# Kernel optimization log

Hardware: AMD Instinct MI355X
Metric: run time of the kernel (lower is better)

Reference implementation:

```python
import jax, jax.numpy as jnp
import numpy as np

EPS = 1e-6                                   # VN leaky-relu denominator eps
BN_SCALE = np.float32(1.0 / np.sqrt(1.0 + 1e-5))  # eval-mode BatchNorm with default stats
NEG = 0.2                                    # negative_slope


def vn_lin(x, w):
    # x: [n, c, 3, ...]; w: [c, o] -> [n, o, 3, ...]
    return jnp.einsum('nc...,co->no...', x, w)


def vn_act(p, d):
    # Vector-Neuron leaky ReLU: project p off the half-space defined by direction d.
    dot = jnp.sum(p * d, axis=2, keepdims=True)
    dsq = jnp.sum(d * d, axis=2, keepdims=True)
    corr = p - (dot / (dsq + EPS)) * d
    return NEG * p + (1.0 - NEG) * jnp.where(dot >= 0, p, corr)


def score_net(x, w_vn, wd_vn, w_h1, w_h2, b_h2, temp=1.0):
    # CorrelationNet: VNLinearLeakyReLU(3 -> 2*ks) -> norm -> 1x1 convs -> softmax
    p = vn_lin(x, w_vn) * BN_SCALE           # [N, 2ks, 3, K] (VNBatchNorm ~ scalar in eval)
    d = vn_lin(x, wd_vn)
    s = vn_act(p, d)
    s = jnp.linalg.norm(s, axis=2)           # [N, 2ks, K]
    s = jax.nn.relu(jnp.einsum('nck,co->nok', s, w_h1) * BN_SCALE)  # conv1d k=1, BN, relu
    s = jnp.einsum('nck,co->nok', s, w_h2) + b_h2[None, :, None]     # last conv with bias
    return jax.nn.softmax(s / temp, axis=1)  # [N, ks, K]


def setup_inputs() -> dict:
    key = jax.random.key(0)
    k = [jax.random.fold_in(key, i) for i in range(13)]
    N, N2, K, KS, OUT = 16000, 20000, 16, 8, 64
    half = OUT // 2
    return {
        'q_pts': jax.random.normal(k[0], (N, 3), jnp.float32),
        's_pts': jax.random.normal(k[1], (N2, 3), jnp.float32),
        's_feats': jax.random.normal(k[2], (N2, 1, 3), jnp.float32),
        'neighbor_indices': jax.random.randint(k[3], (N, K), 0, N2),
        'wb': jax.random.normal(k[4], (3, KS * half), jnp.float32) * np.float32(np.sqrt(2.0 / 3.0)),
        'w_vn': jax.random.normal(k[5], (3, 2 * KS), jnp.float32) * 0.5,
        'wd_vn': jax.random.normal(k[6], (3, 2 * KS), jnp.float32) * 0.5,
        'w_h1': jax.random.normal(k[7], (2 * KS, KS), jnp.float32) * 0.25,
        'w_h2': jax.random.normal(k[8], (KS, KS), jnp.float32) * 0.35,
        'b_h2': jnp.zeros((KS,), jnp.float32),
        'wd_relu': jax.random.normal(k[9], (half, half), jnp.float32) * 0.18,
        'w_un': jax.random.normal(k[10], (half, OUT), jnp.float32) * 0.18,
        'wd_un': jax.random.normal(k[11], (half, OUT), jnp.float32) * 0.18,
    }


def reference(q_pts, s_pts, s_feats, neighbor_indices, wb, w_vn, wd_vn,
              w_h1, w_h2, b_h2, wd_relu, w_un, wd_un):
    N, K = neighbor_indices.shape
    KS = w_h2.shape[1]
    # neighbor gather + centering: [N, K, 3] -> [N, 1, 3, K]
    pts = s_pts[neighbor_indices] - q_pts[:, None]
    pts = jnp.transpose(pts, (0, 2, 1))[:, None]
    centers = jnp.broadcast_to(jnp.mean(pts, axis=-1, keepdims=True), pts.shape)
    cross = jnp.cross(pts, centers, axis=2)
    local = jnp.concatenate([pts, centers, cross], axis=1)   # [N, 3, 3, K]
    scores = score_net(local, w_vn, wd_vn, w_h1, w_h2, b_h2)  # [N, KS, K]
    # kernel-point correlation conv
    pro = jnp.einsum('ncdk,cf->nfdk', local, wb)              # [N, KS*half, 3, K]
    pro = pro.reshape(N, KS, -1, 3, K)
    pro = jnp.sum(pro * scores[:, :, None, None, :], axis=1)  # [N, half, 3, K]
    nrm = jnp.linalg.norm(pro, axis=2, keepdims=True)
    normed = pro / jnp.maximum(nrm, 1e-12)                    # F.normalize(p=2, dim=2)
    feats = jnp.mean(normed, axis=-1)                         # [N, half, 3]
    feats = vn_act(feats, vn_lin(feats, wd_relu))             # VNLeakyReLU
    out = vn_act(vn_lin(feats, w_un) * BN_SCALE, vn_lin(feats, wd_un))  # VNLinearLeakyReLU
    return out                                                # [N, out_dim, 3]
```

## Files before the change

kernel.cpp:

```cpp
#include <hip/hip_runtime.h>
#include <math.h>

#define VN_EPS   1e-6f
#define NEG      0.2f
#define POS      0.8f

typedef float v2f __attribute__((ext_vector_type(2)));
typedef float v4f __attribute__((ext_vector_type(4)));

template <int CTRL>
__device__ __forceinline__ float dpp_add(float v) {
    int s = __builtin_amdgcn_update_dpp(0, __float_as_int(v), CTRL, 0xf, 0xf, true);
    return v + __int_as_float(s);
}
__device__ __forceinline__ float row16_allsum(float v) {
    v = dpp_add<0x128>(v);
    v = dpp_add<0x124>(v);
    v = dpp_add<0x122>(v);
    v = dpp_add<0x121>(v);
    return v;
}
__device__ __forceinline__ float row16_sum15(float v) {
    v = dpp_add<0x118>(v);
    v = dpp_add<0x114>(v);
    v = dpp_add<0x112>(v);
    v = dpp_add<0x111>(v);
    return v;
}
__device__ __forceinline__ float swz_xor16(float v) {
    return __int_as_float(__builtin_amdgcn_ds_swizzle(__float_as_int(v), 0x401F));
}
__device__ __forceinline__ float sum_xor32(float v) {
#if __has_builtin(__builtin_amdgcn_permlane32_swap)
    auto r = __builtin_amdgcn_permlane32_swap(__float_as_uint(v), __float_as_uint(v),
                                              false, false);
    return __uint_as_float(r[0]) + __uint_as_float(r[1]);
#else
    return v + __shfl_xor(v, 32, 64);
#endif
}
__device__ __forceinline__ float og4_reduce(float v) {
    v += swz_xor16(v);
    return sum_xor32(v);
}

__global__ __launch_bounds__(256) void areconv_all(
    const float* __restrict__ q_pts,
    const float* __restrict__ s_pts,
    const int*   __restrict__ nbr,
    const float* __restrict__ wb,
    const float* __restrict__ w_vn,
    const float* __restrict__ wd_vn,
    const float* __restrict__ w_h1,
    const float* __restrict__ w_h2,
    const float* __restrict__ b_h2,
    const float* __restrict__ wd_relu,
    const float* __restrict__ w_un,
    const float* __restrict__ wd_un,
    float* __restrict__ out,
    int N)
{
    const float BN_SCALE = 0.999994993f;

    __shared__ __align__(16) float sw_sc[16][8];
    __shared__ __align__(16) float swh1 [16][8];
    __shared__ __align__(16) float swb  [768];
    __shared__ __align__(16) float sfeat [4][3][32];
    __shared__ __align__(16) float sfeat2[4][3][32];

    const int tid = threadIdx.x;
    if (tid < 128) {
        const int o = tid >> 3, j = tid & 7;
        sw_sc[o][j] = (j < 3) ? w_vn[j * 16 + o]
                    : ((j < 6) ? wd_vn[(j - 3) * 16 + o] : 0.f);
        swh1[o][j] = w_h1[tid];
    }
#pragma unroll
    for (int i = 0; i < 3; ++i) swb[tid + 256 * i] = wb[tid + 256 * i];
    __syncthreads();

    const int wv   = tid >> 6;
    const int lane = tid & 63;
    const int og   = lane >> 4;
    const int k    = lane & 15;
    int n = blockIdx.x * 4 + wv;
    n = (n < N) ? n : (N - 1);

    const float qx = q_pts[n * 3 + 0];
    const float qy = q_pts[n * 3 + 1];
    const float qz = q_pts[n * 3 + 2];
    const int   id = nbr[n * 16 + k];
    const float px = s_pts[id * 3 + 0] - qx;
    const float py = s_pts[id * 3 + 1] - qy;
    const float pz = s_pts[id * 3 + 2] - qz;

    const float cx = row16_allsum(px) * 0.0625f;
    const float cy = row16_allsum(py) * 0.0625f;
    const float cz = row16_allsum(pz) * 0.0625f;

    const float rx = py * cz - pz * cy;
    const float ry = pz * cx - px * cz;
    const float rz = px * cy - py * cx;

    const float L[3][3] = {{px, py, pz}, {cx, cy, cz}, {rx, ry, rz}};

    v4f t0123 = {0.f, 0.f, 0.f, 0.f}, t4567 = t0123;
#pragma unroll 1
    for (int o4 = 0; o4 < 4; ++o4) {
        const int o = og * 4 + o4;
        const v4f wa  = *(const v4f*)&sw_sc[o][0];
        const v2f wb2 = *(const v2f*)&sw_sc[o][4];
        const float wv0 = wa[0], wv1 = wa[1], wv2 = wa[2];
        const float wd0 = wa[3], wd1 = wb2[0], wd2 = wb2[1];
        float pv[3], dv[3];
        float dot = 0.f, dsq = 0.f;
#pragma unroll
        for (int d = 0; d < 3; ++d) {
            const float pp = BN_SCALE * (L[0][d] * wv0 + L[1][d] * wv1 + L[2][d] * wv2);
            const float dd = L[0][d] * wd0 + L[1][d] * wd1 + L[2][d] * wd2;
            pv[d] = pp; dv[d] = dd;
            dot += pp * dd;
            dsq += dd * dd;
        }
        const float f = dot * __builtin_amdgcn_rcpf(dsq + VN_EPS);
        float acc = 0.f;
#pragma unroll
        for (int d = 0; d < 3; ++d) {
            const float corr = pv[d] - f * dv[d];
            const float sel  = (dot >= 0.f) ? pv[d] : corr;
            const float a    = NEG * pv[d] + POS * sel;
            acc += a * a;
        }
        const float s = __builtin_amdgcn_sqrtf(acc);
        t0123 += s * (*(const v4f*)&swh1[o][0]);
        t4567 += s * (*(const v4f*)&swh1[o][4]);
    }
#pragma unroll
    for (int e = 0; e < 4; ++e) {
        t0123[e] = og4_reduce(t0123[e]);
        t4567[e] = og4_reduce(t4567[e]);
    }

    float tt[8];
#pragma unroll
    for (int e = 0; e < 4; ++e) {
        tt[e]     = fmaxf(t0123[e] * BN_SCALE, 0.f);
        tt[4 + e] = fmaxf(t4567[e] * BN_SCALE, 0.f);
    }

    float sc[8];
    float mx = -1e30f;
#pragma unroll
    for (int op = 0; op < 4; ++op) {
        v2f u = *(const v2f*)&b_h2[2 * op];
#pragma unroll
        for (int c = 0; c < 8; ++c)
            u += tt[c] * (*(const v2f*)&w_h2[c * 8 + 2 * op]);
        sc[2 * op + 0] = u[0];
        sc[2 * op + 1] = u[1];
        mx = fmaxf(mx, fmaxf(u[0], u[1]));
    }
    float se = 0.f;
#pragma unroll
    for (int o = 0; o < 8; ++o) { sc[o] = __expf(sc[o] - mx); se += sc[o]; }
    const float inv_se = __builtin_amdgcn_rcpf(se);
#pragma unroll
    for (int o = 0; o < 8; ++o) sc[o] *= inv_se;

#pragma unroll 1
    for (int gi = 0; gi < 2; ++gi) {
        const int hb = og * 8 + gi * 4;
        const float* wp = &swb[hb];
        v4f W0 = sc[0] * (*(const v4f*)&wp[0]);
        v4f W1 = sc[0] * (*(const v4f*)&wp[256]);
        v4f W2 = sc[0] * (*(const v4f*)&wp[512]);
#pragma unroll
        for (int s = 1; s < 8; ++s) {
            const float sv = sc[s];
            W0 += sv * (*(const v4f*)&wp[s * 32]);
            W1 += sv * (*(const v4f*)&wp[256 + s * 32]);
            W2 += sv * (*(const v4f*)&wp[512 + s * 32]);
        }
        v4f V0 = L[0][0] * W0 + L[1][0] * W1 + L[2][0] * W2;
        v4f V1 = L[0][1] * W0 + L[1][1] * W1 + L[2][1] * W2;
        v4f V2 = L[0][2] * W0 + L[1][2] * W1 + L[2][2] * W2;
        const v4f vv = V0 * V0 + V1 * V1 + V2 * V2;
#pragma unroll
        for (int e = 0; e < 4; ++e) {
            const float inn = __builtin_amdgcn_rsqf(fmaxf(vv[e], 1e-24f)) * 0.0625f;
            V0[e] = row16_sum15(V0[e] * inn);
            V1[e] = row16_sum15(V1[e] * inn);
            V2[e] = row16_sum15(V2[e] * inn);
        }
        if (k == 15) {
            *(v4f*)&sfeat[wv][0][hb] = V0;
            *(v4f*)&sfeat[wv][1][hb] = V1;
            *(v4f*)&sfeat[wv][2][hb] = V2;
        }
    }

    const int oo = lane & 31;
    {
        const int hh = (lane >> 5) * 16;
        float D0 = 0.f, D1 = 0.f, D2 = 0.f;
#pragma unroll
        for (int hq = 0; hq < 4; ++hq) {
            const int hb = hh + hq * 4;
            const v4f f0 = *(const v4f*)&sfeat[wv][0][hb];
            const v4f f1 = *(const v4f*)&sfeat[wv][1][hb];
            const v4f f2 = *(const v4f*)&sfeat[wv][2][hb];
#pragma unroll
            for (int e = 0; e < 4; ++e) {
                const float w = wd_relu[(hb + e) * 32 + oo];
                D0 += f0[e] * w;
                D1 += f1[e] * w;
                D2 += f2[e] * w;
            }
        }
        D0 = sum_xor32(D0);
        D1 = sum_xor32(D1);
        D2 = sum_xor32(D2);
        const float p0 = sfeat[wv][0][oo];
        const float p1 = sfeat[wv][1][oo];
        const float p2 = sfeat[wv][2][oo];
        const float dot = p0 * D0 + p1 * D1 + p2 * D2;
        const float dsq = D0 * D0 + D1 * D1 + D2 * D2;
        const float f   = dot * __builtin_amdgcn_rcpf(dsq + VN_EPS);
        const bool  pos = (dot >= 0.f);
        if (lane < 32) {
            sfeat2[wv][0][oo] = NEG * p0 + POS * (pos ? p0 : (p0 - f * D0));
            sfeat2[wv][1][oo] = NEG * p1 + POS * (pos ? p1 : (p1 - f * D1));
            sfeat2[wv][2][oo] = NEG * p2 + POS * (pos ? p2 : (p2 - f * D2));
        }
    }

    {
        float AU0 = 0.f, AU1 = 0.f, AU2 = 0.f;
        float AV0 = 0.f, AV1 = 0.f, AV2 = 0.f;
#pragma unroll 1
        for (int hq = 0; hq < 8; ++hq) {
            const v4f f0 = *(const v4f*)&sfeat2[wv][0][hq * 4];
            const v4f f1 = *(const v4f*)&sfeat2[wv][1][hq * 4];
            const v4f f2 = *(const v4f*)&sfeat2[wv][2][hq * 4];
#pragma unroll
            for (int e = 0; e < 4; ++e) {
                const float wu = w_un [(hq * 4 + e) * 64 + lane];
                const float wd = wd_un[(hq * 4 + e) * 64 + lane];
                AU0 += f0[e] * wu; AU1 += f1[e] * wu; AU2 += f2[e] * wu;
                AV0 += f0[e] * wd; AV1 += f1[e] * wd; AV2 += f2[e] * wd;
            }
        }
        const float u0 = AU0 * BN_SCALE;
        const float u1 = AU1 * BN_SCALE;
        const float u2 = AU2 * BN_SCALE;
        const float dot = u0 * AV0 + u1 * AV1 + u2 * AV2;
        const float dsq = AV0 * AV0 + AV1 * AV1 + AV2 * AV2;
        const float f   = dot * __builtin_amdgcn_rcpf(dsq + VN_EPS);
        const bool  pos = (dot >= 0.f);
        const float O0 = NEG * u0 + POS * (pos ? u0 : (u0 - f * AV0));
        const float O1 = NEG * u1 + POS * (pos ? u1 : (u1 - f * AV1));
        const float O2 = NEG * u2 + POS * (pos ? u2 : (u2 - f * AV2));
        float* dst = out + (long)n * 192 + 3 * lane;
        dst[0] = O0;
        dst[1] = O1;
        dst[2] = O2;
    }
}

extern "C" void kernel_launch(void* const* d_in, const int* in_sizes, int n_in,
                              void* d_out, int out_size, void* d_ws, size_t ws_size,
                              hipStream_t stream) {
    const float* q_pts   = (const float*)d_in[0];
    const float* s_pts   = (const float*)d_in[1];
    const int*   nbr     = (const int*)  d_in[3];
    const float* wb      = (const float*)d_in[4];
    const float* w_vn    = (const float*)d_in[5];
    const float* wd_vn   = (const float*)d_in[6];
    const float* w_h1    = (const float*)d_in[7];
    const float* w_h2    = (const float*)d_in[8];
    const float* b_h2    = (const float*)d_in[9];
    const float* wd_relu = (const float*)d_in[10];
    const float* w_un    = (const float*)d_in[11];
    const float* wd_un   = (const float*)d_in[12];
    float* out = (float*)d_out;

    const int N = in_sizes[0] / 3;
    const int blocks = (N + 3) / 4;
    areconv_all<<<blocks, 256, 0, stream>>>(
        q_pts, s_pts, nbr, wb, w_vn, wd_vn, w_h1, w_h2, b_h2,
        wd_relu, w_un, wd_un, out, N);
}
```

Before: 116.7 us.

## Process two query points per wavefront using half-wave partitions

Remaps the wavefront so each 32-lane half handles its own query point, which doubles the points per block and halves the grid. Each half now does twice as many score channels and hidden groups per lane. In exchange the cross-half permlane reductions disappear and the final linear layer computes two output channels per lane with vectorized loads and stores. Per-lane serial work rises while the total lane count needed drops, so latency hiding and occupancy trade-offs change.

```diff
diff --git a/kernel.cpp b/kernel.cpp
--- a/kernel.cpp
+++ b/kernel.cpp
@@ -29,19 +29,6 @@
 }
 __device__ __forceinline__ float swz_xor16(float v) {
     return __int_as_float(__builtin_amdgcn_ds_swizzle(__float_as_int(v), 0x401F));
-}
-__device__ __forceinline__ float sum_xor32(float v) {
-#if __has_builtin(__builtin_amdgcn_permlane32_swap)
-    auto r = __builtin_amdgcn_permlane32_swap(__float_as_uint(v), __float_as_uint(v),
-                                              false, false);
-    return __uint_as_float(r[0]) + __uint_as_float(r[1]);
-#else
-    return v + __shfl_xor(v, 32, 64);
-#endif
-}
-__device__ __forceinline__ float og4_reduce(float v) {
-    v += swz_xor16(v);
-    return sum_xor32(v);
 }
 
 __global__ __launch_bounds__(256) void areconv_all(
@@ -65,8 +52,8 @@
     __shared__ __align__(16) float sw_sc[16][8];
     __shared__ __align__(16) float swh1 [16][8];
     __shared__ __align__(16) float swb  [768];
-    __shared__ __align__(16) float sfeat [4][3][32];
-    __shared__ __align__(16) float sfeat2[4][3][32];
+    __shared__ __align__(16) float sfeat [8][3][32];
+    __shared__ __align__(16) float sfeat2[8][3][32];
 
     const int tid = threadIdx.x;
     if (tid < 128) {
@@ -81,9 +68,11 @@
 
     const int wv   = tid >> 6;
     const int lane = tid & 63;
-    const int og   = lane >> 4;
+    const int p    = lane >> 5;
+    const int og   = (lane >> 4) & 1;
     const int k    = lane & 15;
-    int n = blockIdx.x * 4 + wv;
+    const int bp   = wv * 2 + p;
+    int n = blockIdx.x * 8 + bp;
     n = (n < N) ? n : (N - 1);
 
     const float qx = q_pts[n * 3 + 0];
@@ -106,8 +95,8 @@
 
     v4f t0123 = {0.f, 0.f, 0.f, 0.f}, t4567 = t0123;
 #pragma unroll 1
-    for (int o4 = 0; o4 < 4; ++o4) {
-        const int o = og * 4 + o4;
+    for (int o8 = 0; o8 < 8; ++o8) {
+        const int o = og * 8 + o8;
         const v4f wa  = *(const v4f*)&sw_sc[o][0];
         const v2f wb2 = *(const v2f*)&sw_sc[o][4];
         const float wv0 = wa[0], wv1 = wa[1], wv2 = wa[2];
@@ -137,8 +126,8 @@
     }
 #pragma unroll
     for (int e = 0; e < 4; ++e) {
-        t0123[e] = og4_reduce(t0123[e]);
-        t4567[e] = og4_reduce(t4567[e]);
+        t0123[e] += swz_xor16(t0123[e]);
+        t4567[e] += swz_xor16(t4567[e]);
     }
 
     float tt[8];
@@ -168,8 +157,8 @@
     for (int o = 0; o < 8; ++o) sc[o] *= inv_se;
 
 #pragma unroll 1
-    for (int gi = 0; gi < 2; ++gi) {
-        const int hb = og * 8 + gi * 4;
+    for (int gi = 0; gi < 4; ++gi) {
+        const int hb = og * 16 + gi * 4;
         const float* wp = &swb[hb];
         v4f W0 = sc[0] * (*(const v4f*)&wp[0]);
         v4f W1 = sc[0] * (*(const v4f*)&wp[256]);
@@ -193,77 +182,75 @@
             V2[e] = row16_sum15(V2[e] * inn);
         }
         if (k == 15) {
-            *(v4f*)&sfeat[wv][0][hb] = V0;
-            *(v4f*)&sfeat[wv][1][hb] = V1;
-            *(v4f*)&sfeat[wv][2][hb] = V2;
+            *(v4f*)&sfeat[bp][0][hb] = V0;
+            *(v4f*)&sfeat[bp][1][hb] = V1;
+            *(v4f*)&sfeat[bp][2][hb] = V2;
         }
     }
 
     const int oo = lane & 31;
     {
-        const int hh = (lane >> 5) * 16;
         float D0 = 0.f, D1 = 0.f, D2 = 0.f;
-#pragma unroll
-        for (int hq = 0; hq < 4; ++hq) {
-            const int hb = hh + hq * 4;
-            const v4f f0 = *(const v4f*)&sfeat[wv][0][hb];
-            const v4f f1 = *(const v4f*)&sfeat[wv][1][hb];
-            const v4f f2 = *(const v4f*)&sfeat[wv][2][hb];
+#pragma unroll 1
+        for (int hq = 0; hq < 8; ++hq) {
+            const v4f f0 = *(const v4f*)&sfeat[bp][0][hq * 4];
+            const v4f f1 = *(const v4f*)&sfeat[bp][1][hq * 4];
+            const v4f f2 = *(const v4f*)&sfeat[bp][2][hq * 4];
 #pragma unroll
             for (int e = 0; e < 4; ++e) {
-                const float w = wd_relu[(hb + e) * 32 + oo];
+                const float w = wd_relu[(hq * 4 + e) * 32 + oo];
                 D0 += f0[e] * w;
                 D1 += f1[e] * w;
                 D2 += f2[e] * w;
             }
         }
-        D0 = sum_xor32(D0);
-        D1 = sum_xor32(D1);
-        D2 = sum_xor32(D2);
-        const float p0 = sfeat[wv][0][oo];
-        const float p1 = sfeat[wv][1][oo];
-        const float p2 = sfeat[wv][2][oo];
+        const float p0 = sfeat[bp][0][oo];
+        const float p1 = sfeat[bp][1][oo];
+        const float p2 = sfeat[bp][2][oo];
         const float dot = p0 * D0 + p1 * D1 + p2 * D2;
         const float dsq = D0 * D0 + D1 * D1 + D2 * D2;
         const float f   = dot * __builtin_amdgcn_rcpf(dsq + VN_EPS);
         const bool  pos = (dot >= 0.f);
-        if (lane < 32) {
-            sfeat2[wv][0][oo] = NEG * p0 + POS * (pos ? p0 : (p0 - f * D0));
-            sfeat2[wv][1][oo] = NEG * p1 + POS * (pos ? p1 : (p1 - f * D1));
-            sfeat2[wv][2][oo] = NEG * p2 + POS * (pos ? p2 : (p2 - f * D2));
-        }
+        sfeat2[bp][0][oo] = NEG * p0 + POS * (pos ? p0 : (p0 - f * D0));
+        sfeat2[bp][1][oo] = NEG * p1 + POS * (pos ? p1 : (p1 - f * D1));
+        sfeat2[bp][2][oo] = NEG * p2 + POS * (pos ? p2 : (p2 - f * D2));
     }
 
     {
-        float AU0 = 0.f, AU1 = 0.f, AU2 = 0.f;
-        float AV0 = 0.f, AV1 = 0.f, AV2 = 0.f;
+        v2f AU0 = {0.f, 0.f}, AU1 = AU0, AU2 = AU0;
+        v2f AV0 = AU0, AV1 = AU0, AV2 = AU0;
 #pragma unroll 1
         for (int hq = 0; hq < 8; ++hq) {
-            const v4f f0 = *(const v4f*)&sfeat2[wv][0][hq * 4];
-            const v4f f1 = *(const v4f*)&sfeat2[wv][1][hq * 4];
-            const v4f f2 = *(const v4f*)&sfeat2[wv][2][hq * 4];
+            const v4f f0 = *(const v4f*)&sfeat2[bp][0][hq * 4];
+            const v4f f1 = *(const v4f*)&sfeat2[bp][1][hq * 4];
+            const v4f f2 = *(const v4f*)&sfeat2[bp][2][hq * 4];
 #pragma unroll
             for (int e = 0; e < 4; ++e) {
-                const float wu = w_un [(hq * 4 + e) * 64 + lane];
-                const float wd = wd_un[(hq * 4 + e) * 64 + lane];
+                const v2f wu = *(const v2f*)&w_un [(hq * 4 + e) * 64 + 2 * oo];
+                const v2f wd = *(const v2f*)&wd_un[(hq * 4 + e) * 64 + 2 * oo];
                 AU0 += f0[e] * wu; AU1 += f1[e] * wu; AU2 += f2[e] * wu;
                 AV0 += f0[e] * wd; AV1 += f1[e] * wd; AV2 += f2[e] * wd;
             }
         }
-        const float u0 = AU0 * BN_SCALE;
-        const float u1 = AU1 * BN_SCALE;
-        const float u2 = AU2 * BN_SCALE;
-        const float dot = u0 * AV0 + u1 * AV1 + u2 * AV2;
-        const float dsq = AV0 * AV0 + AV1 * AV1 + AV2 * AV2;
-        const float f   = dot * __builtin_amdgcn_rcpf(dsq + VN_EPS);
-        const bool  pos = (dot >= 0.f);
-        const float O0 = NEG * u0 + POS * (pos ? u0 : (u0 - f * AV0));
-        const float O1 = NEG * u1 + POS * (pos ? u1 : (u1 - f * AV1));
-        const float O2 = NEG * u2 + POS * (pos ? u2 : (u2 - f * AV2));
-        float* dst = out + (long)n * 192 + 3 * lane;
-        dst[0] = O0;
-        dst[1] = O1;
-        dst[2] = O2;
+        float O[6];
+#pragma unroll
+        for (int j = 0; j < 2; ++j) {
+            const float u0 = AU0[j] * BN_SCALE;
+            const float u1 = AU1[j] * BN_SCALE;
+            const float u2 = AU2[j] * BN_SCALE;
+            const float v0 = AV0[j], v1 = AV1[j], v2 = AV2[j];
+            const float dot = u0 * v0 + u1 * v1 + u2 * v2;
+            const float dsq = v0 * v0 + v1 * v1 + v2 * v2;
+            const float f   = dot * __builtin_amdgcn_rcpf(dsq + VN_EPS);
+            const bool  pos = (dot >= 0.f);
+            O[3 * j + 0] = NEG * u0 + POS * (pos ? u0 : (u0 - f * v0));
+            O[3 * j + 1] = NEG * u1 + POS * (pos ? u1 : (u1 - f * v1));
+            O[3 * j + 2] = NEG * u2 + POS * (pos ? u2 : (u2 - f * v2));
+        }
+        float* dst = out + (long)n * 192 + 6 * oo;
+        *(v2f*)(dst + 0) = *(const v2f*)&O[0];
+        *(v2f*)(dst + 2) = *(const v2f*)&O[2];
+        *(v2f*)(dst + 4) = *(const v2f*)&O[4];
     }
 }
 
@@ -285,7 +272,7 @@
     float* out = (float*)d_out;
 
     const int N = in_sizes[0] / 3;
-    const int blocks = (N + 3) / 4;
+    const int blocks = (N + 7) / 8;
     areconv_all<<<blocks, 256, 0, stream>>>(
         q_pts, s_pts, nbr, wb, w_vn, wd_vn, w_h1, w_h2, b_h2,
         wd_relu, w_un, wd_un, out, N);
```

Measured after the change: 113.7 us. 2.6% less time.
